# Kernel optimization log

Measured on AMD Instinct MI355X. Metric: run time of the kernel, lower is better.

## Reference

```python
import jax, jax.numpy as jnp
import numpy as np

N_NODES = 100000
N_EDGES = 1000000
DIM = 64


def setup_inputs() -> dict:
    key = jax.random.key(0)
    k1, k2, k3 = jax.random.split(key, 3)
    z = jax.random.normal(k1, (N_NODES, DIM), dtype=jnp.float32)
    edge_index = jax.random.randint(k2, (2, N_EDGES), 0, N_NODES, dtype=jnp.int64)
    W = jax.random.normal(k3, (DIM, DIM), dtype=jnp.float32) * 0.01
    bias = jnp.zeros((1,), dtype=jnp.float32)
    return {"z": z, "edge_index": edge_index, "W": W, "bias": bias}


def reference(z, edge_index, W, bias):
    # (z_src @ W * z_dst).sum(-1) + bias
    # Compute z @ W once over nodes (N x dim GEMM), then gather per edge:
    # mathematically identical to gathering first, but avoids an E x dim GEMM.
    zW = z @ W                      # [N, dim]
    src, dst = edge_index[0], edge_index[1]
    scores = jnp.sum(zW[src] * z[dst], axis=1) + bias[0]  # [E]
    return scores
```

## Files before the change

kernel.cpp:

```cpp
#include <hip/hip_runtime.h>

#define DIM 64
#define ROWS 64
#define LROW 72
#define EPAD 72

typedef __attribute__((ext_vector_type(8))) short bf16x8;
typedef __attribute__((ext_vector_type(4))) float f32x4;

__device__ __forceinline__ unsigned short f2bf(float f) {
    unsigned int u = __float_as_uint(f);
    u += 0x7FFFu + ((u >> 16) & 1u);
    return (unsigned short)(u >> 16);
}
__device__ __forceinline__ float bf2f_lo(unsigned int u) {
    return __uint_as_float(u << 16);
}
__device__ __forceinline__ float bf2f_hi(unsigned int u) {
    return __uint_as_float(u & 0xFFFF0000u);
}
__device__ __forceinline__ float dot8_bf16(uint4 a, uint4 b) {
    float p = 0.f;
    p = fmaf(bf2f_lo(a.x), bf2f_lo(b.x), p);
    p = fmaf(bf2f_hi(a.x), bf2f_hi(b.x), p);
    p = fmaf(bf2f_lo(a.y), bf2f_lo(b.y), p);
    p = fmaf(bf2f_hi(a.y), bf2f_hi(b.y), p);
    p = fmaf(bf2f_lo(a.z), bf2f_lo(b.z), p);
    p = fmaf(bf2f_hi(a.z), bf2f_hi(b.z), p);
    p = fmaf(bf2f_lo(a.w), bf2f_lo(b.w), p);
    p = fmaf(bf2f_hi(a.w), bf2f_hi(b.w), p);
    return p;
}
__device__ __forceinline__ float red8(float p) {
    p += __shfl_xor(p, 1);
    p += __shfl_xor(p, 2);
    p += __shfl_xor(p, 4);
    return p;
}

__global__ __launch_bounds__(256) void zw_gemm_mfma_kernel(
    const float* __restrict__ z, const float* __restrict__ W,
    unsigned short* __restrict__ zw_bf, unsigned short* __restrict__ z_bf,
    int n_nodes) {
    __shared__ unsigned short sWt[DIM * LROW];
    __shared__ unsigned short sEpi[4 * 16 * EPAD];

    const int tid  = threadIdx.x;
    const int wave = tid >> 6;
    const int lane = tid & 63;
    const int m    = lane & 15;
    const int quad = lane >> 4;
    const int rowBase = blockIdx.x * ROWS;

    for (int f = tid; f < DIM * DIM; f += 256) {
        const int n = f & 63;
        const int k = f >> 6;
        sWt[n * LROW + k] = f2bf(W[f]);
    }

    const int row = rowBase + wave * 16 + m;
    bf16x8 a0 = {0, 0, 0, 0, 0, 0, 0, 0};
    bf16x8 a1 = {0, 0, 0, 0, 0, 0, 0, 0};
    if (row < n_nodes) {
        const float* zr = z + (size_t)row * DIM + quad * 8;
        float4 v0 = *(const float4*)(zr);
        float4 v1 = *(const float4*)(zr + 4);
        float4 v2 = *(const float4*)(zr + 32);
        float4 v3 = *(const float4*)(zr + 36);
        a0[0] = (short)f2bf(v0.x); a0[1] = (short)f2bf(v0.y);
        a0[2] = (short)f2bf(v0.z); a0[3] = (short)f2bf(v0.w);
        a0[4] = (short)f2bf(v1.x); a0[5] = (short)f2bf(v1.y);
        a0[6] = (short)f2bf(v1.z); a0[7] = (short)f2bf(v1.w);
        a1[0] = (short)f2bf(v2.x); a1[1] = (short)f2bf(v2.y);
        a1[2] = (short)f2bf(v2.z); a1[3] = (short)f2bf(v2.w);
        a1[4] = (short)f2bf(v3.x); a1[5] = (short)f2bf(v3.y);
        a1[6] = (short)f2bf(v3.z); a1[7] = (short)f2bf(v3.w);
        *(bf16x8*)(z_bf + (size_t)row * DIM + quad * 8)      = a0;
        *(bf16x8*)(z_bf + (size_t)row * DIM + 32 + quad * 8) = a1;
    }
    __syncthreads();

    f32x4 acc[4];
#pragma unroll
    for (int t = 0; t < 4; ++t) {
        const unsigned short* bBase = &sWt[(t * 16 + m) * LROW + quad * 8];
        bf16x8 b0 = *(const bf16x8*)(bBase);
        bf16x8 b1 = *(const bf16x8*)(bBase + 32);
        f32x4 c = {0.f, 0.f, 0.f, 0.f};
        c = __builtin_amdgcn_mfma_f32_16x16x32_bf16(a0, b0, c, 0, 0, 0);
        c = __builtin_amdgcn_mfma_f32_16x16x32_bf16(a1, b1, c, 0, 0, 0);
        acc[t] = c;
    }

    unsigned short* ep = &sEpi[wave * 16 * EPAD];
#pragma unroll
    for (int t = 0; t < 4; ++t) {
#pragma unroll
        for (int r = 0; r < 4; ++r) {
            ep[(quad * 4 + r) * EPAD + t * 16 + m] = f2bf(acc[t][r]);
        }
    }
    __syncthreads();
    {
        const int r = lane >> 2;
        const int s = lane & 3;
        const int grow = rowBase + wave * 16 + r;
#pragma unroll
        for (int h = 0; h < 2; ++h) {
            const int seg = h * 4 + s;
            if (grow < n_nodes) {
                bf16x8 v = *(const bf16x8*)(&ep[r * EPAD + seg * 8]);
                *(bf16x8*)(zw_bf + (size_t)grow * DIM + seg * 8) = v;
            }
        }
    }
}

__global__ __launch_bounds__(256) void edge_score_bf16_kernel(
    const unsigned short* __restrict__ zw_bf, const unsigned short* __restrict__ z_bf,
    const int* __restrict__ edge_index, const float* __restrict__ bias,
    float* __restrict__ out, int n_edges) {
    const int tid = blockIdx.x * 256 + threadIdx.x;
    const int group = tid >> 3;
    const int sub = tid & 7;
    const int e0 = group * 4;
    if (e0 >= n_edges) return;

    const float bias0 = bias[0];

    if (e0 + 3 < n_edges) {
        int4 srcs = *(const int4*)(edge_index + e0);
        int4 dsts = *(const int4*)(edge_index + n_edges + e0);

        uint4 a0 = ((const uint4*)(zw_bf + (size_t)srcs.x * DIM))[sub];
        uint4 a1 = ((const uint4*)(zw_bf + (size_t)srcs.y * DIM))[sub];
        uint4 a2 = ((const uint4*)(zw_bf + (size_t)srcs.z * DIM))[sub];
        uint4 a3 = ((const uint4*)(zw_bf + (size_t)srcs.w * DIM))[sub];
        uint4 b0 = ((const uint4*)(z_bf + (size_t)dsts.x * DIM))[sub];
        uint4 b1 = ((const uint4*)(z_bf + (size_t)dsts.y * DIM))[sub];
        uint4 b2 = ((const uint4*)(z_bf + (size_t)dsts.z * DIM))[sub];
        uint4 b3 = ((const uint4*)(z_bf + (size_t)dsts.w * DIM))[sub];

        float p0 = red8(dot8_bf16(a0, b0));
        float p1 = red8(dot8_bf16(a1, b1));
        float p2 = red8(dot8_bf16(a2, b2));
        float p3 = red8(dot8_bf16(a3, b3));

        float v = (sub & 1) ? ((sub & 2) ? p3 : p1) : ((sub & 2) ? p2 : p0);
        if (sub < 4) out[e0 + sub] = v + bias0;
    } else {
        for (int e = e0; e < n_edges; ++e) {
            const int src = edge_index[e];
            const int dst = edge_index[n_edges + e];
            uint4 a = ((const uint4*)(zw_bf + (size_t)src * DIM))[sub];
            uint4 b = ((const uint4*)(z_bf + (size_t)dst * DIM))[sub];
            float p = red8(dot8_bf16(a, b));
            if (sub == 0) out[e] = p + bias0;
        }
    }
}

extern "C" void kernel_launch(void* const* d_in, const int* in_sizes, int n_in,
                              void* d_out, int out_size, void* d_ws, size_t ws_size,
                              hipStream_t stream) {
    const float* z          = (const float*)d_in[0];
    const int*   edge_index = (const int*)d_in[1];
    const float* W          = (const float*)d_in[2];
    const float* bias       = (const float*)d_in[3];
    float* out = (float*)d_out;

    const int n_nodes = in_sizes[0] / DIM;
    const int n_edges = in_sizes[1] / 2;

    unsigned short* zw_bf = (unsigned short*)d_ws;
    unsigned short* z_bf  = zw_bf + (size_t)n_nodes * DIM;

    const int gemm_blocks = (n_nodes + ROWS - 1) / ROWS;
    zw_gemm_mfma_kernel<<<gemm_blocks, 256, 0, stream>>>(z, W, zw_bf, z_bf, n_nodes);

    const int edge_blocks = (n_edges + 127) / 128;
    edge_score_bf16_kernel<<<edge_blocks, 256, 0, stream>>>(zw_bf, z_bf, edge_index,
                                                            bias, out, n_edges);
}
```

Baseline: 116.0 us.

## Switch intermediates from bf16 to fp16 with packed dot2 and larger GEMM tiles

Node features and zW are now stored as fp16 instead of bf16. The conversions use packed cvt_pkrtz, the GEMM uses the fp16 MFMA, and the per-edge dot product uses fdot2 instructions, which removes the manual unpack and FMA chain in the edge kernel. The GEMM block also handles 128 rows, two 16-row tiles per wave, and the epilogue sync is dropped. fp16 has less dynamic range than bf16, which could overflow for large values. The random-gather memory traffic in the edge kernel is unchanged.

```diff
diff --git a/kernel.cpp b/kernel.cpp
--- a/kernel.cpp
+++ b/kernel.cpp
@@ -1,36 +1,45 @@
 #include <hip/hip_runtime.h>
 
 #define DIM 64
-#define ROWS 64
+#define ROWS 128
 #define LROW 72
 #define EPAD 72
 
-typedef __attribute__((ext_vector_type(8))) short bf16x8;
+typedef __attribute__((ext_vector_type(8))) __fp16 half8;
+typedef __attribute__((ext_vector_type(2))) __fp16 half2v;
 typedef __attribute__((ext_vector_type(4))) float f32x4;
 
-__device__ __forceinline__ unsigned short f2bf(float f) {
-    unsigned int u = __float_as_uint(f);
-    u += 0x7FFFu + ((u >> 16) & 1u);
-    return (unsigned short)(u >> 16);
+__device__ __forceinline__ unsigned int pk2(float a, float b) {
+    half2v h = __builtin_amdgcn_cvt_pkrtz(a, b);
+    return __builtin_bit_cast(unsigned int, h);
 }
-__device__ __forceinline__ float bf2f_lo(unsigned int u) {
-    return __uint_as_float(u << 16);
+
+__device__ __forceinline__ float dot8_f16(uint4 a, uint4 b) {
+#if __has_builtin(__builtin_amdgcn_fdot2)
+    half2v ax = __builtin_bit_cast(half2v, a.x), bx = __builtin_bit_cast(half2v, b.x);
+    half2v ay = __builtin_bit_cast(half2v, a.y), by = __builtin_bit_cast(half2v, b.y);
+    half2v az = __builtin_bit_cast(half2v, a.z), bz = __builtin_bit_cast(half2v, b.z);
+    half2v aw = __builtin_bit_cast(half2v, a.w), bw = __builtin_bit_cast(half2v, b.w);
+    float p0 = __builtin_amdgcn_fdot2(ax, bx, 0.f, false);
+    p0 = __builtin_amdgcn_fdot2(ay, by, p0, false);
+    float p1 = __builtin_amdgcn_fdot2(az, bz, 0.f, false);
+    p1 = __builtin_amdgcn_fdot2(aw, bw, p1, false);
+    return p0 + p1;
+#else
+    half2v ah[4] = {__builtin_bit_cast(half2v, a.x), __builtin_bit_cast(half2v, a.y),
+                    __builtin_bit_cast(half2v, a.z), __builtin_bit_cast(half2v, a.w)};
+    half2v bh[4] = {__builtin_bit_cast(half2v, b.x), __builtin_bit_cast(half2v, b.y),
+                    __builtin_bit_cast(half2v, b.z), __builtin_bit_cast(half2v, b.w)};
+    float p = 0.f;
+#pragma unroll
+    for (int i = 0; i < 4; ++i) {
+        p = fmaf((float)ah[i][0], (float)bh[i][0], p);
+        p = fmaf((float)ah[i][1], (float)bh[i][1], p);
+    }
+    return p;
+#endif
 }
-__device__ __forceinline__ float bf2f_hi(unsigned int u) {
-    return __uint_as_float(u & 0xFFFF0000u);
-}
-__device__ __forceinline__ float dot8_bf16(uint4 a, uint4 b) {
-    float p = 0.f;
-    p = fmaf(bf2f_lo(a.x), bf2f_lo(b.x), p);
-    p = fmaf(bf2f_hi(a.x), bf2f_hi(b.x), p);
-    p = fmaf(bf2f_lo(a.y), bf2f_lo(b.y), p);
-    p = fmaf(bf2f_hi(a.y), bf2f_hi(b.y), p);
-    p = fmaf(bf2f_lo(a.z), bf2f_lo(b.z), p);
-    p = fmaf(bf2f_hi(a.z), bf2f_hi(b.z), p);
-    p = fmaf(bf2f_lo(a.w), bf2f_lo(b.w), p);
-    p = fmaf(bf2f_hi(a.w), bf2f_hi(b.w), p);
-    return p;
-}
+
 __device__ __forceinline__ float red8(float p) {
     p += __shfl_xor(p, 1);
     p += __shfl_xor(p, 2);
@@ -40,7 +49,7 @@
 
 __global__ __launch_bounds__(256) void zw_gemm_mfma_kernel(
     const float* __restrict__ z, const float* __restrict__ W,
-    unsigned short* __restrict__ zw_bf, unsigned short* __restrict__ z_bf,
+    unsigned short* __restrict__ zw_h, unsigned short* __restrict__ z_h,
     int n_nodes) {
     __shared__ unsigned short sWt[DIM * LROW];
     __shared__ unsigned short sEpi[4 * 16 * EPAD];
@@ -55,69 +64,71 @@
     for (int f = tid; f < DIM * DIM; f += 256) {
         const int n = f & 63;
         const int k = f >> 6;
-        sWt[n * LROW + k] = f2bf(W[f]);
+        sWt[n * LROW + k] = __builtin_bit_cast(unsigned short, (__fp16)W[f]);
     }
 
-    const int row = rowBase + wave * 16 + m;
-    bf16x8 a0 = {0, 0, 0, 0, 0, 0, 0, 0};
-    bf16x8 a1 = {0, 0, 0, 0, 0, 0, 0, 0};
-    if (row < n_nodes) {
-        const float* zr = z + (size_t)row * DIM + quad * 8;
+    half8 a0[2], a1[2];
+#pragma unroll
+    for (int tt = 0; tt < 2; ++tt) {
+        const int row = rowBase + wave * 32 + tt * 16 + m;
+        const int rc  = row < n_nodes ? row : n_nodes - 1;
+        const float* zr = z + (size_t)rc * DIM + quad * 8;
         float4 v0 = *(const float4*)(zr);
         float4 v1 = *(const float4*)(zr + 4);
         float4 v2 = *(const float4*)(zr + 32);
         float4 v3 = *(const float4*)(zr + 36);
-        a0[0] = (short)f2bf(v0.x); a0[1] = (short)f2bf(v0.y);
-        a0[2] = (short)f2bf(v0.z); a0[3] = (short)f2bf(v0.w);
-        a0[4] = (short)f2bf(v1.x); a0[5] = (short)f2bf(v1.y);
-        a0[6] = (short)f2bf(v1.z); a0[7] = (short)f2bf(v1.w);
-        a1[0] = (short)f2bf(v2.x); a1[1] = (short)f2bf(v2.y);
-        a1[2] = (short)f2bf(v2.z); a1[3] = (short)f2bf(v2.w);
-        a1[4] = (short)f2bf(v3.x); a1[5] = (short)f2bf(v3.y);
-        a1[6] = (short)f2bf(v3.z); a1[7] = (short)f2bf(v3.w);
-        *(bf16x8*)(z_bf + (size_t)row * DIM + quad * 8)      = a0;
-        *(bf16x8*)(z_bf + (size_t)row * DIM + 32 + quad * 8) = a1;
+        uint4 pa, pb;
+        pa.x = pk2(v0.x, v0.y); pa.y = pk2(v0.z, v0.w);
+        pa.z = pk2(v1.x, v1.y); pa.w = pk2(v1.z, v1.w);
+        pb.x = pk2(v2.x, v2.y); pb.y = pk2(v2.z, v2.w);
+        pb.z = pk2(v3.x, v3.y); pb.w = pk2(v3.z, v3.w);
+        a0[tt] = __builtin_bit_cast(half8, pa);
+        a1[tt] = __builtin_bit_cast(half8, pb);
+        if (row < n_nodes) {
+            *(uint4*)(z_h + (size_t)row * DIM + quad * 8)      = pa;
+            *(uint4*)(z_h + (size_t)row * DIM + 32 + quad * 8) = pb;
+        }
     }
     __syncthreads();
 
-    f32x4 acc[4];
+    half8 b0[4], b1[4];
 #pragma unroll
     for (int t = 0; t < 4; ++t) {
         const unsigned short* bBase = &sWt[(t * 16 + m) * LROW + quad * 8];
-        bf16x8 b0 = *(const bf16x8*)(bBase);
-        bf16x8 b1 = *(const bf16x8*)(bBase + 32);
-        f32x4 c = {0.f, 0.f, 0.f, 0.f};
-        c = __builtin_amdgcn_mfma_f32_16x16x32_bf16(a0, b0, c, 0, 0, 0);
-        c = __builtin_amdgcn_mfma_f32_16x16x32_bf16(a1, b1, c, 0, 0, 0);
-        acc[t] = c;
+        b0[t] = *(const half8*)(bBase);
+        b1[t] = *(const half8*)(bBase + 32);
     }
 
     unsigned short* ep = &sEpi[wave * 16 * EPAD];
 #pragma unroll
-    for (int t = 0; t < 4; ++t) {
+    for (int tt = 0; tt < 2; ++tt) {
 #pragma unroll
-        for (int r = 0; r < 4; ++r) {
-            ep[(quad * 4 + r) * EPAD + t * 16 + m] = f2bf(acc[t][r]);
+        for (int t = 0; t < 4; ++t) {
+            f32x4 c = {0.f, 0.f, 0.f, 0.f};
+            c = __builtin_amdgcn_mfma_f32_16x16x32_f16(a0[tt], b0[t], c, 0, 0, 0);
+            c = __builtin_amdgcn_mfma_f32_16x16x32_f16(a1[tt], b1[t], c, 0, 0, 0);
+#pragma unroll
+            for (int r = 0; r < 4; ++r) {
+                ep[(quad * 4 + r) * EPAD + t * 16 + m] =
+                    __builtin_bit_cast(unsigned short, (__fp16)c[r]);
+            }
         }
-    }
-    __syncthreads();
-    {
         const int r = lane >> 2;
         const int s = lane & 3;
-        const int grow = rowBase + wave * 16 + r;
+        const int grow = rowBase + wave * 32 + tt * 16 + r;
 #pragma unroll
         for (int h = 0; h < 2; ++h) {
             const int seg = h * 4 + s;
             if (grow < n_nodes) {
-                bf16x8 v = *(const bf16x8*)(&ep[r * EPAD + seg * 8]);
-                *(bf16x8*)(zw_bf + (size_t)grow * DIM + seg * 8) = v;
+                uint4 v = *(const uint4*)(&ep[r * EPAD + seg * 8]);
+                *(uint4*)(zw_h + (size_t)grow * DIM + seg * 8) = v;
             }
         }
     }
 }
 
-__global__ __launch_bounds__(256) void edge_score_bf16_kernel(
-    const unsigned short* __restrict__ zw_bf, const unsigned short* __restrict__ z_bf,
+__global__ __launch_bounds__(256) void edge_score_f16_kernel(
+    const unsigned short* __restrict__ zw_h, const unsigned short* __restrict__ z_h,
     const int* __restrict__ edge_index, const float* __restrict__ bias,
     float* __restrict__ out, int n_edges) {
     const int tid = blockIdx.x * 256 + threadIdx.x;
@@ -132,19 +143,19 @@
         int4 srcs = *(const int4*)(edge_index + e0);
         int4 dsts = *(const int4*)(edge_index + n_edges + e0);
 
-        uint4 a0 = ((const uint4*)(zw_bf + (size_t)srcs.x * DIM))[sub];
-        uint4 a1 = ((const uint4*)(zw_bf + (size_t)srcs.y * DIM))[sub];
-        uint4 a2 = ((const uint4*)(zw_bf + (size_t)srcs.z * DIM))[sub];
-        uint4 a3 = ((const uint4*)(zw_bf + (size_t)srcs.w * DIM))[sub];
-        uint4 b0 = ((const uint4*)(z_bf + (size_t)dsts.x * DIM))[sub];
-        uint4 b1 = ((const uint4*)(z_bf + (size_t)dsts.y * DIM))[sub];
-        uint4 b2 = ((const uint4*)(z_bf + (size_t)dsts.z * DIM))[sub];
-        uint4 b3 = ((const uint4*)(z_bf + (size_t)dsts.w * DIM))[sub];
+        uint4 a0 = ((const uint4*)(zw_h + (size_t)srcs.x * DIM))[sub];
+        uint4 a1 = ((const uint4*)(zw_h + (size_t)srcs.y * DIM))[sub];
+        uint4 a2 = ((const uint4*)(zw_h + (size_t)srcs.z * DIM))[sub];
+        uint4 a3 = ((const uint4*)(zw_h + (size_t)srcs.w * DIM))[sub];
+        uint4 b0 = ((const uint4*)(z_h + (size_t)dsts.x * DIM))[sub];
+        uint4 b1 = ((const uint4*)(z_h + (size_t)dsts.y * DIM))[sub];
+        uint4 b2 = ((const uint4*)(z_h + (size_t)dsts.z * DIM))[sub];
+        uint4 b3 = ((const uint4*)(z_h + (size_t)dsts.w * DIM))[sub];
 
-        float p0 = red8(dot8_bf16(a0, b0));
-        float p1 = red8(dot8_bf16(a1, b1));
-        float p2 = red8(dot8_bf16(a2, b2));
-        float p3 = red8(dot8_bf16(a3, b3));
+        float p0 = red8(dot8_f16(a0, b0));
+        float p1 = red8(dot8_f16(a1, b1));
+        float p2 = red8(dot8_f16(a2, b2));
+        float p3 = red8(dot8_f16(a3, b3));
 
         float v = (sub & 1) ? ((sub & 2) ? p3 : p1) : ((sub & 2) ? p2 : p0);
         if (sub < 4) out[e0 + sub] = v + bias0;
@@ -152,9 +163,9 @@
         for (int e = e0; e < n_edges; ++e) {
             const int src = edge_index[e];
             const int dst = edge_index[n_edges + e];
-            uint4 a = ((const uint4*)(zw_bf + (size_t)src * DIM))[sub];
-            uint4 b = ((const uint4*)(z_bf + (size_t)dst * DIM))[sub];
-            float p = red8(dot8_bf16(a, b));
+            uint4 a = ((const uint4*)(zw_h + (size_t)src * DIM))[sub];
+            uint4 b = ((const uint4*)(z_h + (size_t)dst * DIM))[sub];
+            float p = red8(dot8_f16(a, b));
             if (sub == 0) out[e] = p + bias0;
         }
     }
@@ -172,13 +183,13 @@
     const int n_nodes = in_sizes[0] / DIM;
     const int n_edges = in_sizes[1] / 2;
 
-    unsigned short* zw_bf = (unsigned short*)d_ws;
-    unsigned short* z_bf  = zw_bf + (size_t)n_nodes * DIM;
+    unsigned short* zw_h = (unsigned short*)d_ws;
+    unsigned short* z_h  = zw_h + (size_t)n_nodes * DIM;
 
     const int gemm_blocks = (n_nodes + ROWS - 1) / ROWS;
-    zw_gemm_mfma_kernel<<<gemm_blocks, 256, 0, stream>>>(z, W, zw_bf, z_bf, n_nodes);
+    zw_gemm_mfma_kernel<<<gemm_blocks, 256, 0, stream>>>(z, W, zw_h, z_h, n_nodes);
 
     const int edge_blocks = (n_edges + 127) / 128;
-    edge_score_bf16_kernel<<<edge_blocks, 256, 0, stream>>>(zw_bf, z_bf, edge_index,
-                                                            bias, out, n_edges);
+    edge_score_f16_kernel<<<edge_blocks, 256, 0, stream>>>(zw_h, z_h, edge_index,
+                                                           bias, out, n_edges);
 }
```

Measured after the change: 115.1 us. No clear change (-0.8%).
